# Kernel tuning notes

Measured on AMD Instinct MI355X. Metric: run time of the kernel, lower is better.

Reference implementation:

```python
import jax, jax.numpy as jnp
import numpy as np

B, S, D = 64, 512, 768   # batch, seq_len, bert hidden
H = D // 2               # per-direction LSTM hidden (384)
T = 9                    # tag_num
L, NDIR = 2, 2           # lstm layers, directions


def setup_inputs() -> dict:
    key = jax.random.key(0)
    ks = jax.random.split(key, 10)
    def n(k, shape, s=0.05):
        return jax.random.normal(k, shape, jnp.float32) * s
    return {
        "bert_output": jax.random.normal(ks[0], (B, S, D), jnp.float32),
        "y": jax.random.randint(ks[1], (B, S), 0, T),
        "lstm_Wih": n(ks[2], (L, NDIR, 4 * H, D)),   # input_size==D for both layers (bi-output = D)
        "lstm_Whh": n(ks[3], (L, NDIR, 4 * H, H)),
        "lstm_b":   n(ks[4], (L, NDIR, 4 * H)),      # b_ih + b_hh fused (mathematically identical)
        "fc_w": n(ks[5], (T, D)),
        "fc_b": n(ks[6], (T,)),
        "trans":   n(ks[7], (T, T), 0.1),
        "start_t": n(ks[8], (T,), 0.1),
        "end_t":   n(ks[9], (T,), 0.1),
    }


def _lstm_dir(x, Wih, Whh, b):
    # x: [B,S,I] -> [B,S,H]; PyTorch gate order i,f,g,o
    Bq, Hq = x.shape[0], Whh.shape[1]
    def step(carry, xt):
        h, c = carry
        g = xt @ Wih.T + h @ Whh.T + b          # [B,4H]
        i, f, gg, o = jnp.split(g, 4, axis=-1)
        c = jax.nn.sigmoid(f) * c + jax.nn.sigmoid(i) * jnp.tanh(gg)
        h = jax.nn.sigmoid(o) * jnp.tanh(c)
        return (h, c), h
    z = jnp.zeros((Bq, Hq), x.dtype)
    _, hs = jax.lax.scan(step, (z, z), jnp.swapaxes(x, 0, 1))
    return jnp.swapaxes(hs, 0, 1)


def _bilstm(x, Wih, Whh, b):
    for l in range(L):
        fwd = _lstm_dir(x, Wih[l, 0], Whh[l, 0], b[l, 0])
        bwd = jnp.flip(_lstm_dir(jnp.flip(x, 1), Wih[l, 1], Whh[l, 1], b[l, 1]), 1)
        x = jnp.concatenate([fwd, bwd], axis=-1)  # [B,S,2H]=[B,S,D]
    return x


def _crf_nll(em, tags, trans, start_t, end_t):
    # em: [B,S,T] emissions; tags: [B,S] int. Negative mean log-likelihood.
    gold = (
        jnp.take_along_axis(em, tags[..., None], axis=-1)[..., 0].sum(-1)
        + trans[tags[:, :-1], tags[:, 1:]].sum(-1)
        + start_t[tags[:, 0]] + end_t[tags[:, -1]]
    )  # [B]
    def step(alpha, em_t):  # alpha,em_t: [B,T]
        a = jax.nn.logsumexp(alpha[:, :, None] + trans[None], axis=1) + em_t
        return a, None
    alpha0 = start_t[None] + em[:, 0]
    alpha, _ = jax.lax.scan(step, alpha0, jnp.swapaxes(em[:, 1:], 0, 1))
    logZ = jax.nn.logsumexp(alpha + end_t[None], axis=-1)  # [B]
    return jnp.mean(logZ - gold)


def _viterbi(em, trans, start_t, end_t):
    def step(v, em_t):
        scores = v[:, :, None] + trans[None]      # [B,Tprev,Tcur]
        bp = jnp.argmax(scores, axis=1)           # [B,T]
        return jnp.max(scores, axis=1) + em_t, bp
    v0 = start_t[None] + em[:, 0]
    v, bps = jax.lax.scan(step, v0, jnp.swapaxes(em[:, 1:], 0, 1))  # bps: [S-1,B,T]
    last = jnp.argmax(v + end_t[None], axis=-1)   # [B]
    def back(tag, bp):
        prev = jnp.take_along_axis(bp, tag[:, None], axis=1)[:, 0]
        return prev, tag
    first, rest = jax.lax.scan(back, last, bps, reverse=True)  # rest: tags at 1..S-1
    tags = jnp.concatenate([first[None], rest], axis=0)        # [S,B]
    return jnp.swapaxes(tags, 0, 1)               # [B,S]


def reference(bert_output, y, lstm_Wih, lstm_Whh, lstm_b, fc_w, fc_b, trans, start_t, end_t):
    h = _bilstm(bert_output, lstm_Wih, lstm_Whh, lstm_b)
    em = h @ fc_w.T + fc_b                        # [B,S,T]
    loss = _crf_nll(em, y, trans, start_t, end_t)
    tag = _viterbi(em, trans, start_t, end_t)
    return (loss, tag)
```

## Files before the change

kernel.cpp:

```cpp
#include <hip/hip_runtime.h>

#define Bn   64
#define Sn   512
#define Dn   768
#define Hn   384
#define G4n  1536
#define Tn   9
#define SCHn 64
#define NCH  8

#define BUFU (2ull * Bn * SCHn * G4n)

#define OFF_WIHB  0ull
#define SZ_WIHB   (2ull * Dn * G4n)
#define OFF_GATESB (OFF_WIHB + SZ_WIHB)
#define SZ_GATESB (4ull * BUFU / 2)
#define OFF_H1B   (OFF_GATESB + SZ_GATESB)
#define SZ_H1B    ((unsigned long long)Bn * Sn * Dn / 2)
#define OFF_BERTB (OFF_H1B + SZ_H1B)
#define SZ_BERTB  ((unsigned long long)Bn * Sn * Dn / 2)
#define OFF_EMP   (OFF_BERTB + SZ_BERTB)
#define SZ_EMP    (2ull * Bn * Sn * Tn)
#define OFF_EM    (OFF_EMP + SZ_EMP)
#define SZ_EM     ((unsigned long long)Bn * Sn * Tn)
#define OFF_HBUF  (OFF_EM + SZ_EM)
#define SZ_HBUF   (8ull * Bn * Hn)
#define OFF_CST   (OFF_HBUF + SZ_HBUF)
#define SZ_CST    (4ull * Bn * Hn)
#define OFF_LP    (OFF_CST + SZ_CST)
#define SZ_LP     64ull
#define OFF_STAMP (OFF_LP + SZ_LP)
#define STAMP_TOTAL (2 * 2 * 8 * 32 * 32)

typedef __attribute__((ext_vector_type(8))) short short8v;
typedef __attribute__((ext_vector_type(4))) float f32x4;

static __device__ __forceinline__ float sigf(float x) { return 1.f / (1.f + expf(-x)); }

static __device__ __forceinline__ unsigned short f2bf(float x) {
    unsigned u = __float_as_uint(x);
    u += 0x7fffu + ((u >> 16) & 1u);
    return (unsigned short)(u >> 16);
}
static __device__ __forceinline__ float bf2f(unsigned short u) {
    return __uint_as_float(((unsigned)u) << 16);
}

static __device__ __forceinline__ unsigned long long llc_load_u64(const unsigned long long* p) {
    return __hip_atomic_load(p, __ATOMIC_RELAXED, __HIP_MEMORY_SCOPE_SYSTEM);
}
static __device__ __forceinline__ void llc_store_f32(float* p, float v) {
    __hip_atomic_store(p, v, __ATOMIC_RELAXED, __HIP_MEMORY_SCOPE_SYSTEM);
}
static __device__ __forceinline__ int llc_load_i32(const int* p) {
    return __hip_atomic_load(p, __ATOMIC_RELAXED, __HIP_MEMORY_SCOPE_SYSTEM);
}

__global__ void to_bf16(const float* __restrict__ in, unsigned short* __restrict__ out,
                        int total)
{
    for (int i = blockIdx.x * 256 + threadIdx.x; i < total; i += gridDim.x * 256)
        out[i] = f2bf(in[i]);
}

__global__ void init_bar(int* __restrict__ st)
{
    const int i = blockIdx.x * 256 + threadIdx.x;
    if (i < STAMP_TOTAL) st[i] = 0;
}

static __device__ __forceinline__ void gemm_tile(
    unsigned short As[][40], unsigned short Bs[][40],
    const unsigned short* __restrict__ Abf,
    const unsigned short* __restrict__ Wb,
    const float* __restrict__ bvec,
    unsigned short* __restrict__ G,
    int layer, int chunk, int nb, int mb, int tid)
{
    const int m0  = mb * 128;
    const int dir = mb >> 5;
    const int n0c = nb * 128;

    const unsigned short* BT = Wb + (size_t)(layer * 2 + dir) * G4n * Dn;
    const float* bias = bvec + (size_t)(layer * 2 + dir) * G4n;

    const int mm   = tid >> 1;
    const int seg  = (tid & 1) * 16;
    const int rem  = (m0 + mm) & (Bn * SCHn - 1);
    const int bb   = rem >> 6;
    const int j    = rem & (SCHn - 1);
    const int p    = chunk * SCHn + j;
    const int s    = dir ? (Sn - 1 - p) : p;
    const unsigned short* arow = Abf + ((size_t)bb * Sn + s) * Dn;
    const unsigned short* brow = BT + (size_t)(n0c + mm) * Dn;

    const int l = tid & 63, wave = tid >> 6;
    const int wy = wave >> 1, wx = wave & 1;
    const int fr = l & 15, fk = (l >> 4) * 8;

    f32x4 acc[4][4];
    #pragma unroll
    for (int mt = 0; mt < 4; ++mt)
        #pragma unroll
        for (int nt = 0; nt < 4; ++nt)
            acc[mt][nt] = (f32x4){0.f, 0.f, 0.f, 0.f};

    for (int k0 = 0; k0 < Dn; k0 += 32) {
        const short8v a0 = *(const short8v*)(arow + k0 + seg);
        const short8v a1 = *(const short8v*)(arow + k0 + seg + 8);
        const short8v b0 = *(const short8v*)(brow + k0 + seg);
        const short8v b1 = *(const short8v*)(brow + k0 + seg + 8);
        __syncthreads();
        *(short8v*)&As[mm][seg]     = a0;
        *(short8v*)&As[mm][seg + 8] = a1;
        *(short8v*)&Bs[mm][seg]     = b0;
        *(short8v*)&Bs[mm][seg + 8] = b1;
        __syncthreads();

        short8v af[4], bf[4];
        #pragma unroll
        for (int mt = 0; mt < 4; ++mt)
            af[mt] = *(const short8v*)&As[wy * 64 + mt * 16 + fr][fk];
        #pragma unroll
        for (int nt = 0; nt < 4; ++nt)
            bf[nt] = *(const short8v*)&Bs[wx * 64 + nt * 16 + fr][fk];
        #pragma unroll
        for (int mt = 0; mt < 4; ++mt)
            #pragma unroll
            for (int nt = 0; nt < 4; ++nt)
                acc[mt][nt] = __builtin_amdgcn_mfma_f32_16x16x32_bf16(
                    af[mt], bf[nt], acc[mt][nt], 0, 0, 0);
    }

    #pragma unroll
    for (int nt = 0; nt < 4; ++nt) {
        const int n  = n0c + wx * 64 + nt * 16 + fr;
        const int g  = n / 384;
        const int d2 = n - g * 384;
        const int gcol = d2 * 4 + g;
        const float bv = bias[n];
        #pragma unroll
        for (int mt = 0; mt < 4; ++mt) {
            #pragma unroll
            for (int q = 0; q < 4; ++q) {
                const int row = m0 + wy * 64 + mt * 16 + (l >> 4) * 4 + q;
                G[(size_t)row * G4n + gcol] = f2bf(acc[mt][nt][q] + bv);
            }
        }
    }
}

__global__ __launch_bounds__(256) void gemm_pair(
    const unsigned short* __restrict__ A0, int l0, int c0, unsigned short* __restrict__ G0,
    const unsigned short* __restrict__ A1, int l1, int c1, unsigned short* __restrict__ G1,
    int valid1,
    const unsigned short* __restrict__ Wb, const float* __restrict__ bvec)
{
    __shared__ __align__(16) unsigned short As[128][40];
    __shared__ __align__(16) unsigned short Bs[128][40];
    if (blockIdx.z == 1) {
        if (!valid1) return;
        gemm_tile(As, Bs, A1, Wb, bvec, G1, l1, c1, blockIdx.x, blockIdx.y, threadIdx.x);
    } else {
        gemm_tile(As, Bs, A0, Wb, bvec, G0, l0, c0, blockIdx.x, blockIdx.y, threadIdx.x);
    }
}

__global__ __launch_bounds__(256, 2) void lstm_dual(
    const unsigned short* __restrict__ grdA, int la, int ca,
    const unsigned short* __restrict__ grdB, int lb, int cb, int validB,
    const float* __restrict__ Whh,
    const float* __restrict__ fcw,
    unsigned short* __restrict__ h1b,
    float* __restrict__ emP,
    float* __restrict__ hbuf,
    float* __restrict__ cst,
    int* __restrict__ stamps)
{
    const int tid = threadIdx.x;
    const int bid = blockIdx.x;
    const int half = bid >> 9;
    if (half && !validB) return;
    const unsigned short* grd = half ? grdB : grdA;
    const int layer = half ? lb : la;
    const int chunk = half ? cb : ca;
    const int lbid = bid & 511;
    const int dir = lbid >> 8;
    const int bg  = (lbid >> 5) & 7;
    const int dg  = lbid & 31;
    const int b0 = bg * 8, d0 = dg * 12;

    __shared__ __align__(16) float hstage[8][396];
    __shared__ __align__(16) float red[4][16][28];
    __shared__ float cs[8][12];
    __shared__ float fcwl[Hn];

    const int ct = tid & 15;
    const int kq = tid >> 4;
    const int k0 = kq * 24;
    const int sbb = tid >> 5, skq = tid & 31;
    const bool pw = (tid < 96);
    const int pb = tid / 12, pdd = tid - pb * 12;
    const int lane = tid & 63, wv = tid >> 6;

    int* lstamps = stamps + layer * (2 * 8 * 32 * 32);
    const int* mystamps = lstamps + ((dir * 8 + bg) * 32 + skq) * 32;
    float* lhbuf = hbuf + (size_t)layer * (4ull * Bn * Hn);
    float* lcst  = cst + (size_t)layer * (2ull * Bn * Hn);

    float wreg[72];
    {
        const float* Wbase = Whh + (size_t)(layer * 2 + dir) * G4n * Hn;
        #pragma unroll
        for (int c = 0; c < 3; ++c) {
            const int cc = ct * 3 + c;
            const int dd = cc >> 2, g = cc & 3;
            const float* wr = Wbase + (size_t)(g * Hn + d0 + dd) * Hn + k0;
            #pragma unroll
            for (int kk = 0; kk < 24; kk += 4) {
                const float4 w4 = *(const float4*)(wr + kk);
                wreg[c * 24 + kk + 0] = w4.x;
                wreg[c * 24 + kk + 1] = w4.y;
                wreg[c * 24 + kk + 2] = w4.z;
                wreg[c * 24 + kk + 3] = w4.w;
            }
        }
    }

    const bool fcwg = (layer == 1) && (dg < Tn);
    if (fcwg) {
        for (int k2 = tid; k2 < Hn; k2 += 256)
            fcwl[k2] = fcw[dg * Dn + dir * Hn + k2];
    }

    if (pw) {
        cs[pb][pdd] = (chunk == 0) ? 0.f
            : lcst[((size_t)dir * Bn + b0 + pb) * Hn + d0 + pdd];
    }
    __syncthreads();

    for (int j = 0; j < SCHn; ++j) {
        const int sg = chunk * SCHn + j;
        const int p_rd = sg & 1, p_wr = (sg + 1) & 1;
        const int s = dir ? (Sn - 1 - sg) : sg;

        float4 g4 = make_float4(0.f, 0.f, 0.f, 0.f);
        if (pw) {
            const ushort4 gu = *(const ushort4*)(grd +
                  (((size_t)(dir * Bn + b0 + pb) * SCHn + j) * G4n) + (d0 + pdd) * 4);
            g4.x = bf2f(gu.x); g4.y = bf2f(gu.y);
            g4.z = bf2f(gu.z); g4.w = bf2f(gu.w);
        }

        if (chunk == 0 && j == 0) {
            #pragma unroll
            for (int i = 0; i < 6; ++i)
                *(float2*)&hstage[sbb][skq * 12 + 2 * i] = make_float2(0.f, 0.f);
        } else {
            const int need = sg;
            while (llc_load_i32(mystamps) < need) __builtin_amdgcn_s_sleep(1);
            const unsigned long long* hsrc = (const unsigned long long*)
                (lhbuf + ((size_t)(p_rd * 2 + dir) * Bn + b0 + sbb) * Hn) + skq * 6;
            #pragma unroll
            for (int i = 0; i < 6; ++i) {
                const unsigned long long v = llc_load_u64(hsrc + i);
                float2 f2;
                f2.x = __uint_as_float((unsigned int)v);
                f2.y = __uint_as_float((unsigned int)(v >> 32));
                *(float2*)&hstage[sbb][skq * 12 + 2 * i] = f2;
            }
        }
        __syncthreads();

        float acc[24];
        #pragma unroll
        for (int i = 0; i < 24; ++i) acc[i] = 0.f;
        #pragma unroll
        for (int b = 0; b < 8; ++b) {
            const float* hp = &hstage[b][k0];
            float hv[24];
            #pragma unroll
            for (int i = 0; i < 6; ++i) {
                const float4 h4 = *(const float4*)(hp + i * 4);
                hv[i * 4 + 0] = h4.x; hv[i * 4 + 1] = h4.y;
                hv[i * 4 + 2] = h4.z; hv[i * 4 + 3] = h4.w;
            }
            #pragma unroll
            for (int c = 0; c < 3; ++c)
                #pragma unroll
                for (int kk = 0; kk < 24; ++kk)
                    acc[b * 3 + c] += hv[kk] * wreg[c * 24 + kk];
        }
        #pragma unroll
        for (int i = 0; i < 24; ++i) {
            acc[i] += __shfl_xor(acc[i], 16);
            acc[i] += __shfl_xor(acc[i], 32);
        }
        if (lane < 16) {
            #pragma unroll
            for (int i = 0; i < 24; i += 4) {
                float4 t4; t4.x = acc[i]; t4.y = acc[i + 1];
                t4.z = acc[i + 2]; t4.w = acc[i + 3];
                *(float4*)&red[wv][lane][i] = t4;
            }
        }

        if (fcwg && j >= 1) {
            const int sgp = sg - 1;
            const int sprev = dir ? (Sn - 1 - sgp) : sgp;
            const float* hp2 = &hstage[sbb][skq * 12];
            const float* wp2 = &fcwl[skq * 12];
            float e2 = 0.f;
            #pragma unroll
            for (int q = 0; q < 12; ++q) e2 += hp2[q] * wp2[q];
            e2 += __shfl_down(e2, 16, 32);
            e2 += __shfl_down(e2, 8, 32);
            e2 += __shfl_down(e2, 4, 32);
            e2 += __shfl_down(e2, 2, 32);
            e2 += __shfl_down(e2, 1, 32);
            if (skq == 0)
                emP[((size_t)(dir * Bn + b0 + sbb) * Sn + sprev) * Tn + dg] = e2;
        }
        __syncthreads();

        if (pw) {
            float pre[4];
            #pragma unroll
            for (int g = 0; g < 4; ++g) {
                const int cc = pdd * 4 + g;
                const int ct2 = cc / 3;
                const int e = pb * 3 + (cc - ct2 * 3);
                pre[g] = red[0][ct2][e] + red[1][ct2][e]
                       + red[2][ct2][e] + red[3][ct2][e];
            }
            const float ii = sigf(pre[0] + g4.x);
            const float ff = sigf(pre[1] + g4.y);
            const float gg = tanhf(pre[2] + g4.z);
            const float oo = sigf(pre[3] + g4.w);
            const float cn = ff * cs[pb][pdd] + ii * gg;
            cs[pb][pdd] = cn;
            const float hn = oo * tanhf(cn);
            llc_store_f32(&lhbuf[((size_t)(p_wr * 2 + dir) * Bn + b0 + pb) * Hn + d0 + pdd], hn);
            if (layer == 0)
                h1b[((size_t)(b0 + pb) * Sn + s) * Dn + dir * Hn + d0 + pdd] = f2bf(hn);
        }
        __syncthreads();
        if (tid == 0)
            __hip_atomic_store(lstamps + ((dir * 8 + bg) * 32 + dg) * 32, sg + 1,
                               __ATOMIC_RELAXED, __HIP_MEMORY_SCOPE_SYSTEM);
    }

    if (fcwg) {
        const int sgl = chunk * SCHn + SCHn - 1;
        const int need = sgl + 1;
        while (llc_load_i32(mystamps) < need) __builtin_amdgcn_s_sleep(1);
        const int pp = (sgl + 1) & 1;
        const unsigned long long* hsrc = (const unsigned long long*)
            (lhbuf + ((size_t)(pp * 2 + dir) * Bn + b0 + sbb) * Hn) + skq * 6;
        #pragma unroll
        for (int i = 0; i < 6; ++i) {
            const unsigned long long v = llc_load_u64(hsrc + i);
            float2 f2;
            f2.x = __uint_as_float((unsigned int)v);
            f2.y = __uint_as_float((unsigned int)(v >> 32));
            *(float2*)&hstage[sbb][skq * 12 + 2 * i] = f2;
        }
        __syncthreads();
        const int sprev = dir ? (Sn - 1 - sgl) : sgl;
        const float* hp2 = &hstage[sbb][skq * 12];
        const float* wp2 = &fcwl[skq * 12];
        float e2 = 0.f;
        #pragma unroll
        for (int q = 0; q < 12; ++q) e2 += hp2[q] * wp2[q];
        e2 += __shfl_down(e2, 16, 32);
        e2 += __shfl_down(e2, 8, 32);
        e2 += __shfl_down(e2, 4, 32);
        e2 += __shfl_down(e2, 2, 32);
        e2 += __shfl_down(e2, 1, 32);
        if (skq == 0)
            emP[((size_t)(dir * Bn + b0 + sbb) * Sn + sprev) * Tn + dg] = e2;
    }

    if (pw)
        lcst[((size_t)dir * Bn + b0 + pb) * Hn + d0 + pdd] = cs[pb][pdd];
}

__global__ void em_combine(const float* __restrict__ emP, const float* __restrict__ fcb,
                           float* __restrict__ em)
{
    const int idx = blockIdx.x * 256 + threadIdx.x;
    if (idx < Bn * Sn * Tn) {
        const int t = idx % Tn;
        em[idx] = emP[idx] + emP[(size_t)Bn * Sn * Tn + idx] + fcb[t];
    }
}

__global__ __launch_bounds__(64) void crf_loss(
    const float* __restrict__ em, const int* __restrict__ y,
    const float* __restrict__ trans, const float* __restrict__ start_t,
    const float* __restrict__ end_t, float* __restrict__ lossp)
{
    const int b = blockIdx.x, tid = threadIdx.x;
    __shared__ float tr[Tn * Tn];
    for (int i = tid; i < Tn * Tn; i += 64) tr[i] = trans[i];
    __syncthreads();
    const int* yb = y + (size_t)b * Sn;
    const float* emb = em + (size_t)b * Sn * Tn;

    float gs = 0.f;
    for (int s2 = tid; s2 < Sn; s2 += 64) gs += emb[s2 * Tn + yb[s2]];
    for (int s2 = tid; s2 < Sn - 1; s2 += 64) gs += tr[yb[s2] * Tn + yb[s2 + 1]];
    #pragma unroll
    for (int o = 32; o > 0; o >>= 1) gs += __shfl_down(gs, o, 64);

    const int jj = (tid < Tn) ? tid : 0;
    float alpha = start_t[jj] + emb[jj];
    for (int s2 = 1; s2 < Sn; ++s2) {
        float av[Tn];
        #pragma unroll
        for (int i = 0; i < Tn; ++i) av[i] = __shfl(alpha, i, 64) + tr[i * Tn + jj];
        float m = av[0];
        #pragma unroll
        for (int i = 1; i < Tn; ++i) m = fmaxf(m, av[i]);
        float ss = 0.f;
        #pragma unroll
        for (int i = 0; i < Tn; ++i) ss += expf(av[i] - m);
        alpha = logf(ss) + m + emb[s2 * Tn + jj];
    }
    const float xv = alpha + end_t[jj];
    float m9 = -1e30f, vv[Tn];
    #pragma unroll
    for (int i = 0; i < Tn; ++i) { vv[i] = __shfl(xv, i, 64); m9 = fmaxf(m9, vv[i]); }
    float s9 = 0.f;
    #pragma unroll
    for (int i = 0; i < Tn; ++i) s9 += expf(vv[i] - m9);
    const float logZ = logf(s9) + m9;
    if (tid == 0) lossp[b] = logZ - (gs + start_t[yb[0]] + end_t[yb[Sn - 1]]);
}

__global__ __launch_bounds__(64) void loss_final(const float* __restrict__ lossp,
                                                 float* __restrict__ out)
{
    float v = lossp[threadIdx.x];
    #pragma unroll
    for (int o = 32; o > 0; o >>= 1) v += __shfl_down(v, o, 64);
    if (threadIdx.x == 0) out[0] = v * (1.f / 64.f);
}

__global__ __launch_bounds__(64) void viterbi_k(
    const float* __restrict__ em, const float* __restrict__ trans,
    const float* __restrict__ start_t, const float* __restrict__ end_t,
    float* __restrict__ out)
{
    const int b = blockIdx.x, tid = threadIdx.x;
    __shared__ float tr[Tn * Tn];
    __shared__ unsigned char bp[Sn - 1][16];
    __shared__ float vfin[Tn];
    for (int i = tid; i < Tn * Tn; i += 64) tr[i] = trans[i];
    __syncthreads();
    const float* emb = em + (size_t)b * Sn * Tn;
    const int jj = (tid < Tn) ? tid : 0;
    float v = start_t[jj] + emb[jj];
    for (int s2 = 1; s2 < Sn; ++s2) {
        float vv[Tn];
        #pragma unroll
        for (int i = 0; i < Tn; ++i) vv[i] = __shfl(v, i, 64);
        float best = -1e30f; int bi = 0;
        #pragma unroll
        for (int i = 0; i < Tn; ++i) {
            const float sc = vv[i] + tr[i * Tn + jj];
            if (sc > best) { best = sc; bi = i; }
        }
        if (tid < Tn) bp[s2 - 1][tid] = (unsigned char)bi;
        v = best + emb[s2 * Tn + jj];
    }
    if (tid < Tn) vfin[tid] = v + end_t[tid];
    __syncthreads();
    if (tid == 0) {
        float best = -1e30f; int cur = 0;
        for (int i = 0; i < Tn; ++i) if (vfin[i] > best) { best = vfin[i]; cur = i; }
        float* ob = out + 1 + (size_t)b * Sn;
        ob[Sn - 1] = (float)cur;
        for (int s2 = Sn - 1; s2 >= 1; --s2) { cur = bp[s2 - 1][cur]; ob[s2 - 1] = (float)cur; }
    }
}

extern "C" void kernel_launch(void* const* d_in, const int* in_sizes, int n_in,
                              void* d_out, int out_size, void* d_ws, size_t ws_size,
                              hipStream_t stream)
{
    (void)in_sizes; (void)n_in; (void)out_size; (void)ws_size;
    const float* bert  = (const float*)d_in[0];
    const int*   y     = (const int*)d_in[1];
    const float* Wih   = (const float*)d_in[2];
    const float* Whh   = (const float*)d_in[3];
    const float* bvec  = (const float*)d_in[4];
    const float* fcw   = (const float*)d_in[5];
    const float* fcb   = (const float*)d_in[6];
    const float* trans = (const float*)d_in[7];
    const float* stt   = (const float*)d_in[8];
    const float* ent   = (const float*)d_in[9];
    float* out = (float*)d_out;
    float* ws  = (float*)d_ws;

    unsigned short* Wihb   = (unsigned short*)(ws + OFF_WIHB);
    unsigned short* gatesb = (unsigned short*)(ws + OFF_GATESB);
    unsigned short* h1b    = (unsigned short*)(ws + OFF_H1B);
    unsigned short* bertb  = (unsigned short*)(ws + OFF_BERTB);
    float* emP   = ws + OFF_EMP;
    float* em    = ws + OFF_EM;
    float* hbuf  = ws + OFF_HBUF;
    float* cst   = ws + OFF_CST;
    float* lossp = ws + OFF_LP;
    int*   stamps = (int*)(ws + OFF_STAMP);

    init_bar<<<dim3((STAMP_TOTAL + 255) / 256), dim3(256), 0, stream>>>(stamps);
    to_bf16<<<dim3(2048), dim3(256), 0, stream>>>(Wih, Wihb, 4 * G4n * Dn);
    to_bf16<<<dim3(2048), dim3(256), 0, stream>>>(bert, bertb, Bn * Sn * Dn);

    #define GBUF(l, c) (gatesb + (size_t)((l) * 2 + ((c) & 1)) * BUFU)

    gemm_pair<<<dim3(12, 64, 2), dim3(256), 0, stream>>>(
        bertb, 0, 0, GBUF(0, 0), bertb, 0, 0, GBUF(0, 0), 0, Wihb, bvec);

    for (int k = 0; k <= 8; ++k) {
        int la, ca, lb = 1, cb = k - 1;
        int validB = (k >= 1 && k - 1 <= 7) ? 1 : 0;
        if (k <= 7) { la = 0; ca = k; }
        else       { la = 1; ca = 7; validB = 0; }
        lstm_dual<<<dim3(1024), dim3(256), 0, stream>>>(
            GBUF(la, ca), la, ca,
            validB ? GBUF(lb, cb) : GBUF(la, ca), lb, cb, validB,
            Whh, fcw, h1b, emP, hbuf, cst, stamps);

        if (k <= 6) {
            gemm_pair<<<dim3(12, 64, 2), dim3(256), 0, stream>>>(
                bertb, 0, k + 1, GBUF(0, k + 1),
                h1b, 1, k, GBUF(1, k), 1, Wihb, bvec);
        } else if (k == 7) {
            gemm_pair<<<dim3(12, 64, 2), dim3(256), 0, stream>>>(
                h1b, 1, 7, GBUF(1, 7), h1b, 1, 7, GBUF(1, 7), 0, Wihb, bvec);
        }
    }

    em_combine<<<dim3((Bn * Sn * Tn + 255) / 256), dim3(256), 0, stream>>>(emP, fcb, em);
    crf_loss<<<dim3(Bn), dim3(64), 0, stream>>>(em, y, trans, stt, ent, lossp);
    loss_final<<<dim3(1), dim3(64), 0, stream>>>(lossp, out);
    viterbi_k<<<dim3(Bn), dim3(64), 0, stream>>>(em, trans, stt, ent, out);
}
```

Measured before the change: 8.907 ms.

## Pack both LSTM layers into one block and store recurrent weights as bf16

Recurrent weights Whh are converted to bf16 once, and each thread keeps packed bf16 pairs in registers, unpacking them to float for the FMAs. This halves the per-thread weight footprint, which allows each 256-thread block to hold two 128-thread halves, one for the layer-0 chunk and one for the layer-1 chunk. The grid shrinks from 1024 to 512 blocks, so all persistent blocks can be co-resident with fewer per-block reductions. The cost is bf16 rounding of Whh, more K work per thread (48 instead of 24), a wait on two stamp slots, and shared __syncthreads coupling between the two layers' halves.

```diff
diff --git a/kernel.cpp b/kernel.cpp
--- a/kernel.cpp
+++ b/kernel.cpp
@@ -13,7 +13,9 @@
 
 #define OFF_WIHB  0ull
 #define SZ_WIHB   (2ull * Dn * G4n)
-#define OFF_GATESB (OFF_WIHB + SZ_WIHB)
+#define OFF_WHHB  (OFF_WIHB + SZ_WIHB)
+#define SZ_WHHB   (2ull * Hn * G4n)
+#define OFF_GATESB (OFF_WHHB + SZ_WHHB)
 #define SZ_GATESB (4ull * BUFU / 2)
 #define OFF_H1B   (OFF_GATESB + SZ_GATESB)
 #define SZ_H1B    ((unsigned long long)Bn * Sn * Dn / 2)
@@ -45,6 +47,12 @@
 static __device__ __forceinline__ float bf2f(unsigned short u) {
     return __uint_as_float(((unsigned)u) << 16);
 }
+static __device__ __forceinline__ float bflo(unsigned u) {
+    return __uint_as_float(u << 16);
+}
+static __device__ __forceinline__ float bfhi(unsigned u) {
+    return __uint_as_float(u & 0xffff0000u);
+}
 
 static __device__ __forceinline__ unsigned long long llc_load_u64(const unsigned long long* p) {
     return __hip_atomic_load(p, __ATOMIC_RELAXED, __HIP_MEMORY_SCOPE_SYSTEM);
@@ -169,7 +177,7 @@
 __global__ __launch_bounds__(256, 2) void lstm_dual(
     const unsigned short* __restrict__ grdA, int la, int ca,
     const unsigned short* __restrict__ grdB, int lb, int cb, int validB,
-    const float* __restrict__ Whh,
+    const unsigned short* __restrict__ Whhb,
     const float* __restrict__ fcw,
     unsigned short* __restrict__ h1b,
     float* __restrict__ emP,
@@ -179,62 +187,64 @@
 {
     const int tid = threadIdx.x;
     const int bid = blockIdx.x;
-    const int half = bid >> 9;
-    if (half && !validB) return;
-    const unsigned short* grd = half ? grdB : grdA;
-    const int layer = half ? lb : la;
-    const int chunk = half ? cb : ca;
-    const int lbid = bid & 511;
-    const int dir = lbid >> 8;
-    const int bg  = (lbid >> 5) & 7;
-    const int dg  = lbid & 31;
+    const int dir = bid >> 8;
+    const int bg  = (bid >> 5) & 7;
+    const int dg  = bid & 31;
     const int b0 = bg * 8, d0 = dg * 12;
 
-    __shared__ __align__(16) float hstage[8][396];
-    __shared__ __align__(16) float red[4][16][28];
-    __shared__ float cs[8][12];
-    __shared__ float fcwl[Hn];
-
-    const int ct = tid & 15;
-    const int kq = tid >> 4;
-    const int k0 = kq * 24;
-    const int sbb = tid >> 5, skq = tid & 31;
-    const bool pw = (tid < 96);
-    const int pb = tid / 12, pdd = tid - pb * 12;
-    const int lane = tid & 63, wv = tid >> 6;
+    const int T = tid >> 7;
+    const int t = tid & 127;
+    const int valid = T ? validB : 1;
+    const int layer = T ? lb : la;
+    const int chunk = T ? cb : ca;
+    const unsigned short* grd = T ? grdB : grdA;
+
+    __shared__ __align__(16) float hstage[2][8][396];
+    __shared__ __align__(16) float red[2][2][16][28];
+    __shared__ float cs[2][8][12];
+    __shared__ float fcwl[2][Hn];
+
+    const int ct = t & 15;
+    const int kq = t >> 4;
+    const int k0 = kq * 48;
+    const int sbb = t >> 4;
+    const int skq = t & 15;
+    const bool pw = (t < 96);
+    const int pb = t / 12, pdd = t - pb * 12;
+    const int w = (t >> 6) & 1;
 
     int* lstamps = stamps + layer * (2 * 8 * 32 * 32);
-    const int* mystamps = lstamps + ((dir * 8 + bg) * 32 + skq) * 32;
+    const int* sp0 = lstamps + ((dir * 8 + bg) * 32 + 2 * skq) * 32;
+    const int* sp1 = sp0 + 32;
     float* lhbuf = hbuf + (size_t)layer * (4ull * Bn * Hn);
     float* lcst  = cst + (size_t)layer * (2ull * Bn * Hn);
 
-    float wreg[72];
-    {
-        const float* Wbase = Whh + (size_t)(layer * 2 + dir) * G4n * Hn;
+    unsigned wregp[72];
+    if (valid) {
+        const unsigned short* Wbase = Whhb + (size_t)(layer * 2 + dir) * G4n * Hn;
         #pragma unroll
         for (int c = 0; c < 3; ++c) {
             const int cc = ct * 3 + c;
             const int dd = cc >> 2, g = cc & 3;
-            const float* wr = Wbase + (size_t)(g * Hn + d0 + dd) * Hn + k0;
-            #pragma unroll
-            for (int kk = 0; kk < 24; kk += 4) {
-                const float4 w4 = *(const float4*)(wr + kk);
-                wreg[c * 24 + kk + 0] = w4.x;
-                wreg[c * 24 + kk + 1] = w4.y;
-                wreg[c * 24 + kk + 2] = w4.z;
-                wreg[c * 24 + kk + 3] = w4.w;
-            }
-        }
-    }
-
-    const bool fcwg = (layer == 1) && (dg < Tn);
+            const uint4* wr = (const uint4*)(Wbase + (size_t)(g * Hn + d0 + dd) * Hn + k0);
+            #pragma unroll
+            for (int q = 0; q < 6; ++q) {
+                const uint4 v = wr[q];
+                wregp[c * 24 + q * 4 + 0] = v.x;
+                wregp[c * 24 + q * 4 + 1] = v.y;
+                wregp[c * 24 + q * 4 + 2] = v.z;
+                wregp[c * 24 + q * 4 + 3] = v.w;
+            }
+        }
+    }
+
+    const bool fcwg = valid && (layer == 1) && (dg < Tn);
     if (fcwg) {
-        for (int k2 = tid; k2 < Hn; k2 += 256)
-            fcwl[k2] = fcw[dg * Dn + dir * Hn + k2];
-    }
-
-    if (pw) {
-        cs[pb][pdd] = (chunk == 0) ? 0.f
+        for (int k2 = t; k2 < Hn; k2 += 128)
+            fcwl[T][k2] = fcw[dg * Dn + dir * Hn + k2];
+    }
+    if (valid && pw) {
+        cs[T][pb][pdd] = (chunk == 0) ? 0.f
             : lcst[((size_t)dir * Bn + b0 + pb) * Hn + d0 + pdd];
     }
     __syncthreads();
@@ -245,107 +255,117 @@
         const int s = dir ? (Sn - 1 - sg) : sg;
 
         float4 g4 = make_float4(0.f, 0.f, 0.f, 0.f);
-        if (pw) {
-            const ushort4 gu = *(const ushort4*)(grd +
-                  (((size_t)(dir * Bn + b0 + pb) * SCHn + j) * G4n) + (d0 + pdd) * 4);
-            g4.x = bf2f(gu.x); g4.y = bf2f(gu.y);
-            g4.z = bf2f(gu.z); g4.w = bf2f(gu.w);
-        }
-
-        if (chunk == 0 && j == 0) {
-            #pragma unroll
-            for (int i = 0; i < 6; ++i)
-                *(float2*)&hstage[sbb][skq * 12 + 2 * i] = make_float2(0.f, 0.f);
-        } else {
-            const int need = sg;
-            while (llc_load_i32(mystamps) < need) __builtin_amdgcn_s_sleep(1);
-            const unsigned long long* hsrc = (const unsigned long long*)
-                (lhbuf + ((size_t)(p_rd * 2 + dir) * Bn + b0 + sbb) * Hn) + skq * 6;
-            #pragma unroll
-            for (int i = 0; i < 6; ++i) {
-                const unsigned long long v = llc_load_u64(hsrc + i);
-                float2 f2;
-                f2.x = __uint_as_float((unsigned int)v);
-                f2.y = __uint_as_float((unsigned int)(v >> 32));
-                *(float2*)&hstage[sbb][skq * 12 + 2 * i] = f2;
+        if (valid) {
+            if (pw) {
+                const ushort4 gu = *(const ushort4*)(grd +
+                      (((size_t)(dir * Bn + b0 + pb) * SCHn + j) * G4n) + (d0 + pdd) * 4);
+                g4.x = bf2f(gu.x); g4.y = bf2f(gu.y);
+                g4.z = bf2f(gu.z); g4.w = bf2f(gu.w);
+            }
+            if (chunk == 0 && j == 0) {
+                #pragma unroll
+                for (int i = 0; i < 6; ++i)
+                    *(float4*)&hstage[T][sbb][skq * 24 + 4 * i] =
+                        make_float4(0.f, 0.f, 0.f, 0.f);
+            } else {
+                const int need = sg;
+                while (llc_load_i32(sp0) < need || llc_load_i32(sp1) < need)
+                    __builtin_amdgcn_s_sleep(1);
+                const unsigned long long* hsrc = (const unsigned long long*)
+                    (lhbuf + ((size_t)(p_rd * 2 + dir) * Bn + b0 + sbb) * Hn) + skq * 12;
+                #pragma unroll
+                for (int i = 0; i < 6; ++i) {
+                    const unsigned long long v0 = llc_load_u64(hsrc + 2 * i);
+                    const unsigned long long v1 = llc_load_u64(hsrc + 2 * i + 1);
+                    float4 f;
+                    f.x = __uint_as_float((unsigned)v0);
+                    f.y = __uint_as_float((unsigned)(v0 >> 32));
+                    f.z = __uint_as_float((unsigned)v1);
+                    f.w = __uint_as_float((unsigned)(v1 >> 32));
+                    *(float4*)&hstage[T][sbb][skq * 24 + 4 * i] = f;
+                }
             }
         }
         __syncthreads();
 
-        float acc[24];
-        #pragma unroll
-        for (int i = 0; i < 24; ++i) acc[i] = 0.f;
-        #pragma unroll
-        for (int b = 0; b < 8; ++b) {
-            const float* hp = &hstage[b][k0];
-            float hv[24];
-            #pragma unroll
-            for (int i = 0; i < 6; ++i) {
-                const float4 h4 = *(const float4*)(hp + i * 4);
-                hv[i * 4 + 0] = h4.x; hv[i * 4 + 1] = h4.y;
-                hv[i * 4 + 2] = h4.z; hv[i * 4 + 3] = h4.w;
-            }
-            #pragma unroll
-            for (int c = 0; c < 3; ++c)
+        if (valid) {
+            float acc[24];
+            #pragma unroll
+            for (int i = 0; i < 24; ++i) acc[i] = 0.f;
+            #pragma unroll
+            for (int i = 0; i < 12; ++i) {
+                float wf[12];
                 #pragma unroll
-                for (int kk = 0; kk < 24; ++kk)
-                    acc[b * 3 + c] += hv[kk] * wreg[c * 24 + kk];
-        }
-        #pragma unroll
-        for (int i = 0; i < 24; ++i) {
-            acc[i] += __shfl_xor(acc[i], 16);
-            acc[i] += __shfl_xor(acc[i], 32);
-        }
-        if (lane < 16) {
-            #pragma unroll
-            for (int i = 0; i < 24; i += 4) {
-                float4 t4; t4.x = acc[i]; t4.y = acc[i + 1];
-                t4.z = acc[i + 2]; t4.w = acc[i + 3];
-                *(float4*)&red[wv][lane][i] = t4;
-            }
-        }
-
-        if (fcwg && j >= 1) {
-            const int sgp = sg - 1;
-            const int sprev = dir ? (Sn - 1 - sgp) : sgp;
-            const float* hp2 = &hstage[sbb][skq * 12];
-            const float* wp2 = &fcwl[skq * 12];
-            float e2 = 0.f;
-            #pragma unroll
-            for (int q = 0; q < 12; ++q) e2 += hp2[q] * wp2[q];
-            e2 += __shfl_down(e2, 16, 32);
-            e2 += __shfl_down(e2, 8, 32);
-            e2 += __shfl_down(e2, 4, 32);
-            e2 += __shfl_down(e2, 2, 32);
-            e2 += __shfl_down(e2, 1, 32);
-            if (skq == 0)
-                emP[((size_t)(dir * Bn + b0 + sbb) * Sn + sprev) * Tn + dg] = e2;
+                for (int c = 0; c < 3; ++c) {
+                    const unsigned u0 = wregp[c * 24 + 2 * i];
+                    const unsigned u1 = wregp[c * 24 + 2 * i + 1];
+                    wf[c * 4 + 0] = bflo(u0); wf[c * 4 + 1] = bfhi(u0);
+                    wf[c * 4 + 2] = bflo(u1); wf[c * 4 + 3] = bfhi(u1);
+                }
+                #pragma unroll
+                for (int b = 0; b < 8; ++b) {
+                    const float4 h4 = *(const float4*)&hstage[T][b][k0 + 4 * i];
+                    acc[b * 3 + 0] += h4.x * wf[0] + h4.y * wf[1]
+                                    + h4.z * wf[2] + h4.w * wf[3];
+                    acc[b * 3 + 1] += h4.x * wf[4] + h4.y * wf[5]
+                                    + h4.z * wf[6] + h4.w * wf[7];
+                    acc[b * 3 + 2] += h4.x * wf[8] + h4.y * wf[9]
+                                    + h4.z * wf[10] + h4.w * wf[11];
+                }
+            }
+            #pragma unroll
+            for (int i = 0; i < 24; ++i) {
+                acc[i] += __shfl_xor(acc[i], 16);
+                acc[i] += __shfl_xor(acc[i], 32);
+            }
+            if ((t & 63) < 16) {
+                #pragma unroll
+                for (int i = 0; i < 24; i += 4) {
+                    float4 t4; t4.x = acc[i]; t4.y = acc[i + 1];
+                    t4.z = acc[i + 2]; t4.w = acc[i + 3];
+                    *(float4*)&red[T][w][t & 15][i] = t4;
+                }
+            }
+            if (fcwg && j >= 1) {
+                const int sgp = sg - 1;
+                const int sprev = dir ? (Sn - 1 - sgp) : sgp;
+                const float* hp2 = &hstage[T][sbb][skq * 24];
+                const float* wp2 = &fcwl[T][skq * 24];
+                float e2 = 0.f;
+                #pragma unroll
+                for (int q = 0; q < 24; ++q) e2 += hp2[q] * wp2[q];
+                e2 += __shfl_down(e2, 8, 16);
+                e2 += __shfl_down(e2, 4, 16);
+                e2 += __shfl_down(e2, 2, 16);
+                e2 += __shfl_down(e2, 1, 16);
+                if (skq == 0)
+                    emP[((size_t)(dir * Bn + b0 + sbb) * Sn + sprev) * Tn + dg] = e2;
+            }
         }
         __syncthreads();
 
-        if (pw) {
+        if (valid && pw) {
             float pre[4];
             #pragma unroll
             for (int g = 0; g < 4; ++g) {
                 const int cc = pdd * 4 + g;
                 const int ct2 = cc / 3;
                 const int e = pb * 3 + (cc - ct2 * 3);
-                pre[g] = red[0][ct2][e] + red[1][ct2][e]
-                       + red[2][ct2][e] + red[3][ct2][e];
+                pre[g] = red[T][0][ct2][e] + red[T][1][ct2][e];
             }
             const float ii = sigf(pre[0] + g4.x);
             const float ff = sigf(pre[1] + g4.y);
             const float gg = tanhf(pre[2] + g4.z);
             const float oo = sigf(pre[3] + g4.w);
-            const float cn = ff * cs[pb][pdd] + ii * gg;
-            cs[pb][pdd] = cn;
+            const float cn = ff * cs[T][pb][pdd] + ii * gg;
+            cs[T][pb][pdd] = cn;
             const float hn = oo * tanhf(cn);
             llc_store_f32(&lhbuf[((size_t)(p_wr * 2 + dir) * Bn + b0 + pb) * Hn + d0 + pdd], hn);
             if (layer == 0)
                 h1b[((size_t)(b0 + pb) * Sn + s) * Dn + dir * Hn + d0 + pdd] = f2bf(hn);
         }
         __syncthreads();
-        if (tid == 0)
+        if (valid && t == 0)
             __hip_atomic_store(lstamps + ((dir * 8 + bg) * 32 + dg) * 32, sg + 1,
                                __ATOMIC_RELAXED, __HIP_MEMORY_SCOPE_SYSTEM);
     }
@@ -353,36 +373,33 @@
     if (fcwg) {
         const int sgl = chunk * SCHn + SCHn - 1;
         const int need = sgl + 1;
-        while (llc_load_i32(mystamps) < need) __builtin_amdgcn_s_sleep(1);
         const int pp = (sgl + 1) & 1;
+        while (llc_load_i32(sp0) < need || llc_load_i32(sp1) < need)
+            __builtin_amdgcn_s_sleep(1);
         const unsigned long long* hsrc = (const unsigned long long*)
-            (lhbuf + ((size_t)(pp * 2 + dir) * Bn + b0 + sbb) * Hn) + skq * 6;
-        #pragma unroll
-        for (int i = 0; i < 6; ++i) {
+            (lhbuf + ((size_t)(pp * 2 + dir) * Bn + b0 + sbb) * Hn) + skq * 12;
+        float hv[24];
+        #pragma unroll
+        for (int i = 0; i < 12; ++i) {
             const unsigned long long v = llc_load_u64(hsrc + i);
-            float2 f2;
-            f2.x = __uint_as_float((unsigned int)v);
-            f2.y = __uint_as_float((unsigned int)(v >> 32));
-            *(float2*)&hstage[sbb][skq * 12 + 2 * i] = f2;
-        }
-        __syncthreads();
+            hv[2 * i]     = __uint_as_float((unsigned)v);
+            hv[2 * i + 1] = __uint_as_float((unsigned)(v >> 32));
+        }
+        const float* wp2 = &fcwl[T][skq * 24];
+        float e2 = 0.f;
+        #pragma unroll
+        for (int q = 0; q < 24; ++q) e2 += hv[q] * wp2[q];
+        e2 += __shfl_down(e2, 8, 16);
+        e2 += __shfl_down(e2, 4, 16);
+        e2 += __shfl_down(e2, 2, 16);
+        e2 += __shfl_down(e2, 1, 16);
         const int sprev = dir ? (Sn - 1 - sgl) : sgl;
-        const float* hp2 = &hstage[sbb][skq * 12];
-        const float* wp2 = &fcwl[skq * 12];
-        float e2 = 0.f;
-        #pragma unroll
-        for (int q = 0; q < 12; ++q) e2 += hp2[q] * wp2[q];
-        e2 += __shfl_down(e2, 16, 32);
-        e2 += __shfl_down(e2, 8, 32);
-        e2 += __shfl_down(e2, 4, 32);
-        e2 += __shfl_down(e2, 2, 32);
-        e2 += __shfl_down(e2, 1, 32);
         if (skq == 0)
             emP[((size_t)(dir * Bn + b0 + sbb) * Sn + sprev) * Tn + dg] = e2;
     }
 
-    if (pw)
-        lcst[((size_t)dir * Bn + b0 + pb) * Hn + d0 + pdd] = cs[pb][pdd];
+    if (valid && pw)
+        lcst[((size_t)dir * Bn + b0 + pb) * Hn + d0 + pdd] = cs[T][pb][pdd];
 }
 
 __global__ void em_combine(const float* __restrict__ emP, const float* __restrict__ fcb,
@@ -504,6 +521,7 @@
     float* ws  = (float*)d_ws;
 
     unsigned short* Wihb   = (unsigned short*)(ws + OFF_WIHB);
+    unsigned short* Whhb   = (unsigned short*)(ws + OFF_WHHB);
     unsigned short* gatesb = (unsigned short*)(ws + OFF_GATESB);
     unsigned short* h1b    = (unsigned short*)(ws + OFF_H1B);
     unsigned short* bertb  = (unsigned short*)(ws + OFF_BERTB);
@@ -516,6 +534,7 @@
 
     init_bar<<<dim3((STAMP_TOTAL + 255) / 256), dim3(256), 0, stream>>>(stamps);
     to_bf16<<<dim3(2048), dim3(256), 0, stream>>>(Wih, Wihb, 4 * G4n * Dn);
+    to_bf16<<<dim3(1024), dim3(256), 0, stream>>>(Whh, Whhb, 4 * G4n * Hn);
     to_bf16<<<dim3(2048), dim3(256), 0, stream>>>(bert, bertb, Bn * Sn * Dn);
 
     #define GBUF(l, c) (gatesb + (size_t)((l) * 2 + ((c) & 1)) * BUFU)
@@ -528,10 +547,10 @@
         int validB = (k >= 1 && k - 1 <= 7) ? 1 : 0;
         if (k <= 7) { la = 0; ca = k; }
         else       { la = 1; ca = 7; validB = 0; }
-        lstm_dual<<<dim3(1024), dim3(256), 0, stream>>>(
+        lstm_dual<<<dim3(512), dim3(256), 0, stream>>>(
             GBUF(la, ca), la, ca,
             validB ? GBUF(lb, cb) : GBUF(la, ca), lb, cb, validB,
-            Whh, fcw, h1b, emP, hbuf, cst, stamps);
+            Whhb, fcw, h1b, emP, hbuf, cst, stamps);
 
         if (k <= 6) {
             gemm_pair<<<dim3(12, 64, 2), dim3(256), 0, stream>>>(
```

After: 30.66 ms. 3.44x slower.

## Double batch rows per LSTM block, halving block count and stamp groups

Applied to the files above, without the earlier changes.

Each persistent LSTM recurrence block now handles 16 batch rows instead of 8, so the grid shrinks from 1024 to 512 blocks and each block reuses its register-resident Whh slice over twice as many rows. The stamp groups are halved, and each thread now waits on two producer stamps and loads 24 hidden values. The hidden-state staging is padded to avoid LDS bank conflicts, and the final emission dot product reads from registers, which drops one barrier. The aim is to cut the cross-block synchronisation and hidden-state traffic per step. In exchange each block does twice the FMA work and holds more accumulators with the min-blocks hint removed, which may add register spills and lengthen every serial timestep.

```diff
diff --git a/kernel.cpp b/kernel.cpp
--- a/kernel.cpp
+++ b/kernel.cpp
@@ -30,7 +30,8 @@
 #define OFF_LP    (OFF_CST + SZ_CST)
 #define SZ_LP     64ull
 #define OFF_STAMP (OFF_LP + SZ_LP)
-#define STAMP_TOTAL (2 * 2 * 8 * 32 * 32)
+#define STAMP_PER_L (2 * 4 * 32 * 32)
+#define STAMP_TOTAL (2 * STAMP_PER_L)
 
 typedef __attribute__((ext_vector_type(8))) short short8v;
 typedef __attribute__((ext_vector_type(4))) float f32x4;
@@ -166,7 +167,7 @@
     }
 }
 
-__global__ __launch_bounds__(256, 2) void lstm_dual(
+__global__ __launch_bounds__(256) void lstm_dual(
     const unsigned short* __restrict__ grdA, int la, int ca,
     const unsigned short* __restrict__ grdB, int lb, int cb, int validB,
     const float* __restrict__ Whh,
@@ -179,32 +180,35 @@
 {
     const int tid = threadIdx.x;
     const int bid = blockIdx.x;
-    const int half = bid >> 9;
+    const int half = bid >> 8;
     if (half && !validB) return;
     const unsigned short* grd = half ? grdB : grdA;
     const int layer = half ? lb : la;
     const int chunk = half ? cb : ca;
-    const int lbid = bid & 511;
-    const int dir = lbid >> 8;
-    const int bg  = (lbid >> 5) & 7;
+    const int lbid = bid & 255;
+    const int dir = lbid >> 7;
+    const int bg  = (lbid >> 5) & 3;
     const int dg  = lbid & 31;
-    const int b0 = bg * 8, d0 = dg * 12;
-
-    __shared__ __align__(16) float hstage[8][396];
-    __shared__ __align__(16) float red[4][16][28];
-    __shared__ float cs[8][12];
+    const int b0 = bg * 16, d0 = dg * 12;
+
+    __shared__ __align__(16) float hstage[16][452];
+    __shared__ __align__(16) float red[4][16][52];
+    __shared__ float cs[16][12];
     __shared__ float fcwl[Hn];
 
     const int ct = tid & 15;
     const int kq = tid >> 4;
     const int k0 = kq * 24;
-    const int sbb = tid >> 5, skq = tid & 31;
-    const bool pw = (tid < 96);
+    const int sbb = tid >> 4;
+    const int skq = tid & 15;
+    const bool pw = (tid < 192);
     const int pb = tid / 12, pdd = tid - pb * 12;
     const int lane = tid & 63, wv = tid >> 6;
 
-    int* lstamps = stamps + layer * (2 * 8 * 32 * 32);
-    const int* mystamps = lstamps + ((dir * 8 + bg) * 32 + skq) * 32;
+    int* lstamps = stamps + layer * STAMP_PER_L;
+    int* grpbase = lstamps + ((dir * 4 + bg) * 32) * 32;
+    const int* sp0 = grpbase + (2 * skq) * 32;
+    const int* sp1 = grpbase + (2 * skq + 1) * 32;
     float* lhbuf = hbuf + (size_t)layer * (4ull * Bn * Hn);
     float* lcst  = cst + (size_t)layer * (2ull * Bn * Hn);
 
@@ -255,33 +259,35 @@
         if (chunk == 0 && j == 0) {
             #pragma unroll
             for (int i = 0; i < 6; ++i)
-                *(float2*)&hstage[sbb][skq * 12 + 2 * i] = make_float2(0.f, 0.f);
+                *(float4*)&hstage[sbb][skq * 28 + 4 * i] =
+                    make_float4(0.f, 0.f, 0.f, 0.f);
         } else {
             const int need = sg;
-            while (llc_load_i32(mystamps) < need) __builtin_amdgcn_s_sleep(1);
+            while (llc_load_i32(sp0) < need || llc_load_i32(sp1) < need)
+                __builtin_amdgcn_s_sleep(1);
             const unsigned long long* hsrc = (const unsigned long long*)
-                (lhbuf + ((size_t)(p_rd * 2 + dir) * Bn + b0 + sbb) * Hn) + skq * 6;
-            #pragma unroll
-            for (int i = 0; i < 6; ++i) {
+                (lhbuf + ((size_t)(p_rd * 2 + dir) * Bn + b0 + sbb) * Hn) + skq * 12;
+            #pragma unroll
+            for (int i = 0; i < 12; ++i) {
                 const unsigned long long v = llc_load_u64(hsrc + i);
                 float2 f2;
                 f2.x = __uint_as_float((unsigned int)v);
                 f2.y = __uint_as_float((unsigned int)(v >> 32));
-                *(float2*)&hstage[sbb][skq * 12 + 2 * i] = f2;
+                *(float2*)&hstage[sbb][skq * 28 + 2 * i] = f2;
             }
         }
         __syncthreads();
 
-        float acc[24];
-        #pragma unroll
-        for (int i = 0; i < 24; ++i) acc[i] = 0.f;
-        #pragma unroll
-        for (int b = 0; b < 8; ++b) {
-            const float* hp = &hstage[b][k0];
+        float acc[48];
+        #pragma unroll
+        for (int i = 0; i < 48; ++i) acc[i] = 0.f;
+        const float* hrow = &hstage[0][kq * 28];
+        #pragma unroll
+        for (int b = 0; b < 16; ++b) {
             float hv[24];
             #pragma unroll
             for (int i = 0; i < 6; ++i) {
-                const float4 h4 = *(const float4*)(hp + i * 4);
+                const float4 h4 = *(const float4*)(hrow + b * 452 + i * 4);
                 hv[i * 4 + 0] = h4.x; hv[i * 4 + 1] = h4.y;
                 hv[i * 4 + 2] = h4.z; hv[i * 4 + 3] = h4.w;
             }
@@ -292,13 +298,13 @@
                     acc[b * 3 + c] += hv[kk] * wreg[c * 24 + kk];
         }
         #pragma unroll
-        for (int i = 0; i < 24; ++i) {
+        for (int i = 0; i < 48; ++i) {
             acc[i] += __shfl_xor(acc[i], 16);
             acc[i] += __shfl_xor(acc[i], 32);
         }
         if (lane < 16) {
             #pragma unroll
-            for (int i = 0; i < 24; i += 4) {
+            for (int i = 0; i < 48; i += 4) {
                 float4 t4; t4.x = acc[i]; t4.y = acc[i + 1];
                 t4.z = acc[i + 2]; t4.w = acc[i + 3];
                 *(float4*)&red[wv][lane][i] = t4;
@@ -308,16 +314,15 @@
         if (fcwg && j >= 1) {
             const int sgp = sg - 1;
             const int sprev = dir ? (Sn - 1 - sgp) : sgp;
-            const float* hp2 = &hstage[sbb][skq * 12];
-            const float* wp2 = &fcwl[skq * 12];
+            const float* hp2 = &hstage[sbb][skq * 28];
+            const float* wp2 = &fcwl[skq * 24];
             float e2 = 0.f;
             #pragma unroll
-            for (int q = 0; q < 12; ++q) e2 += hp2[q] * wp2[q];
-            e2 += __shfl_down(e2, 16, 32);
-            e2 += __shfl_down(e2, 8, 32);
-            e2 += __shfl_down(e2, 4, 32);
-            e2 += __shfl_down(e2, 2, 32);
-            e2 += __shfl_down(e2, 1, 32);
+            for (int q = 0; q < 24; ++q) e2 += hp2[q] * wp2[q];
+            e2 += __shfl_down(e2, 8, 16);
+            e2 += __shfl_down(e2, 4, 16);
+            e2 += __shfl_down(e2, 2, 16);
+            e2 += __shfl_down(e2, 1, 16);
             if (skq == 0)
                 emP[((size_t)(dir * Bn + b0 + sbb) * Sn + sprev) * Tn + dg] = e2;
         }
@@ -346,37 +351,34 @@
         }
         __syncthreads();
         if (tid == 0)
-            __hip_atomic_store(lstamps + ((dir * 8 + bg) * 32 + dg) * 32, sg + 1,
+            __hip_atomic_store(grpbase + dg * 32, sg + 1,
                                __ATOMIC_RELAXED, __HIP_MEMORY_SCOPE_SYSTEM);
     }
 
     if (fcwg) {
         const int sgl = chunk * SCHn + SCHn - 1;
         const int need = sgl + 1;
-        while (llc_load_i32(mystamps) < need) __builtin_amdgcn_s_sleep(1);
+        while (llc_load_i32(sp0) < need || llc_load_i32(sp1) < need)
+            __builtin_amdgcn_s_sleep(1);
         const int pp = (sgl + 1) & 1;
         const unsigned long long* hsrc = (const unsigned long long*)
-            (lhbuf + ((size_t)(pp * 2 + dir) * Bn + b0 + sbb) * Hn) + skq * 6;
-        #pragma unroll
-        for (int i = 0; i < 6; ++i) {
+            (lhbuf + ((size_t)(pp * 2 + dir) * Bn + b0 + sbb) * Hn) + skq * 12;
+        float hv[24];
+        #pragma unroll
+        for (int i = 0; i < 12; ++i) {
             const unsigned long long v = llc_load_u64(hsrc + i);
-            float2 f2;
-            f2.x = __uint_as_float((unsigned int)v);
-            f2.y = __uint_as_float((unsigned int)(v >> 32));
-            *(float2*)&hstage[sbb][skq * 12 + 2 * i] = f2;
-        }
-        __syncthreads();
+            hv[2 * i]     = __uint_as_float((unsigned int)v);
+            hv[2 * i + 1] = __uint_as_float((unsigned int)(v >> 32));
+        }
+        const float* wp2 = &fcwl[skq * 24];
+        float e2 = 0.f;
+        #pragma unroll
+        for (int q = 0; q < 24; ++q) e2 += hv[q] * wp2[q];
+        e2 += __shfl_down(e2, 8, 16);
+        e2 += __shfl_down(e2, 4, 16);
+        e2 += __shfl_down(e2, 2, 16);
+        e2 += __shfl_down(e2, 1, 16);
         const int sprev = dir ? (Sn - 1 - sgl) : sgl;
-        const float* hp2 = &hstage[sbb][skq * 12];
-        const float* wp2 = &fcwl[skq * 12];
-        float e2 = 0.f;
-        #pragma unroll
-        for (int q = 0; q < 12; ++q) e2 += hp2[q] * wp2[q];
-        e2 += __shfl_down(e2, 16, 32);
-        e2 += __shfl_down(e2, 8, 32);
-        e2 += __shfl_down(e2, 4, 32);
-        e2 += __shfl_down(e2, 2, 32);
-        e2 += __shfl_down(e2, 1, 32);
         if (skq == 0)
             emP[((size_t)(dir * Bn + b0 + sbb) * Sn + sprev) * Tn + dg] = e2;
     }
@@ -528,7 +530,7 @@
         int validB = (k >= 1 && k - 1 <= 7) ? 1 : 0;
         if (k <= 7) { la = 0; ca = k; }
         else       { la = 1; ca = 7; validB = 0; }
-        lstm_dual<<<dim3(1024), dim3(256), 0, stream>>>(
+        lstm_dual<<<dim3(512), dim3(256), 0, stream>>>(
             GBUF(la, ca), la, ca,
             validB ? GBUF(lb, cb) : GBUF(la, ca), lb, cb, validB,
             Whh, fcw, h1b, emP, hbuf, cst, stamps);
```

Result: slower. 10.01 ms (+12.4%).
